# Kernel optimization log

Hardware: AMD Instinct MI355X
Metric: run time of the kernel (lower is better)

Reference implementation:

```python
import jax, jax.numpy as jnp
import numpy as np

HIDDEN = 1024
N_HEADS = 16
HEAD_DIM = HIDDEN // N_HEADS  # 64
B, N = 2, 2048
SCALE = HIDDEN ** (-0.5)  # NOTE: original scales by full hidden_size, not head_dim


def setup_inputs() -> dict:
    key = jax.random.key(0)
    k1, k2 = jax.random.split(key)
    hidden_states = jax.random.normal(k1, (B, N, HIDDEN), dtype=jnp.float32)
    attention_mask = jnp.ones((B, N), dtype=jnp.int32)
    # per-head no-bias Linear(hidden -> 3*head_dim), stacked: [h, hidden, 3*head_dim]
    W_qkv = jax.random.normal(k2, (N_HEADS, HIDDEN, 3 * HEAD_DIM), dtype=jnp.float32) * (HIDDEN ** -0.5)
    return {"hidden_states": hidden_states, "attention_mask": attention_mask, "W_qkv": W_qkv}


def reference(hidden_states, attention_mask, W_qkv):
    # qkv: [b, h, n, 3*d]
    qkv = jnp.einsum('bnD,hDe->bhne', hidden_states, W_qkv)
    q, k, v = jnp.split(qkv, 3, axis=-1)  # each [b, h, n, d]
    scores = jnp.einsum('bhid,bhjd->bhij', q, k) * SCALE
    mask = attention_mask[:, None, None, :] == 0  # [b,1,1,n]
    scores = jnp.where(mask, -jnp.inf, scores)
    attn = jax.nn.softmax(scores, axis=-1)
    out = jnp.einsum('bhij,bhjd->bhid', attn, v)  # [b, h, n, d]
    # rearrange 'b h n d -> b n (h d)'
    return jnp.transpose(out, (0, 2, 1, 3)).reshape(out.shape[0], out.shape[2], -1)
```

## Files before the change

kernel.cpp:

```cpp
#include <hip/hip_runtime.h>
#include <hip/hip_bf16.h>


#define NH   16
#define HD   64
#define SEQ  2048
#define HID  1024
#define E3   192
#define QSCALE 0.04508422017f
#define MBIAS  -43.2808512f

typedef __attribute__((ext_vector_type(8))) short short8;
typedef __attribute__((ext_vector_type(4))) float f32x4;
typedef __attribute__((ext_vector_type(16))) float f32x16;
typedef unsigned short ushort_t;

#define MFMA16(a, b, c) __builtin_amdgcn_mfma_f32_16x16x32_bf16((a), (b), (c), 0, 0, 0)
#define MFMA32(a, b, c) __builtin_amdgcn_mfma_f32_32x32x16_bf16((a), (b), (c), 0, 0, 0)

#if __has_builtin(__builtin_amdgcn_exp2f)
#define EXP2(x) __builtin_amdgcn_exp2f(x)
#else
#define EXP2(x) exp2f(x)
#endif

static __device__ __forceinline__ ushort_t f2bf(float x) {
    unsigned u = __builtin_bit_cast(unsigned, x);
    unsigned r = u + 0x7fff + ((u >> 16) & 1);
    return (ushort_t)(r >> 16);
}

static __device__ __forceinline__ unsigned pack_trunc(float hi, float lo) {
#if __has_builtin(__builtin_amdgcn_perm)
    return __builtin_amdgcn_perm(__builtin_bit_cast(unsigned, hi),
                                 __builtin_bit_cast(unsigned, lo), 0x07060302u);
#else
    return (__builtin_bit_cast(unsigned, hi) & 0xffff0000u) |
           (__builtin_bit_cast(unsigned, lo) >> 16);
#endif
}

static __device__ __forceinline__ void load_lds16(const void* g, void* l) {
    __builtin_amdgcn_global_load_lds(
        (__attribute__((address_space(1))) void*)(g),
        (__attribute__((address_space(3))) void*)(l), 16, 0, 0);
}

__global__ __launch_bounds__(256) void k_cvt_x(const void* __restrict__ Xv,
                                               ushort_t* __restrict__ Xb,
                                               int* __restrict__ flagp) {
    __shared__ int cnt;
    if (threadIdx.x == 0) cnt = 0;
    __syncthreads();
    const unsigned* X32 = (const unsigned*)Xv;
    if (threadIdx.x < 64) {
        unsigned u = X32[(size_t)blockIdx.x * 2048 + threadIdx.x * 32 + 7];
        int bexp = (u >> 7) & 0xFF;
        if (bexp >= 0x68 && bexp <= 0x90) atomicAdd(&cnt, 1);
    }
    __syncthreads();
    const int isf32 = (cnt < 32);
    if (blockIdx.x == 0 && threadIdx.x == 0) *flagp = isf32;

    const size_t base = ((size_t)blockIdx.x * 256 + threadIdx.x) * 16;
    if (isf32) {
        const float* Xf = (const float*)Xv;
        ushort_t tmp[16];
#pragma unroll
        for (int c = 0; c < 4; ++c) {
            float4 v = *(const float4*)(Xf + base + c * 4);
            tmp[c * 4 + 0] = f2bf(v.x); tmp[c * 4 + 1] = f2bf(v.y);
            tmp[c * 4 + 2] = f2bf(v.z); tmp[c * 4 + 3] = f2bf(v.w);
        }
        *(float4*)(Xb + base)     = ((const float4*)tmp)[0];
        *(float4*)(Xb + base + 8) = ((const float4*)tmp)[1];
    } else {
        const ushort_t* Xh = (const ushort_t*)Xv;
        *(float4*)(Xb + base)     = *(const float4*)(Xh + base);
        *(float4*)(Xb + base + 8) = *(const float4*)(Xh + base + 8);
    }
}

__global__ __launch_bounds__(256) void k_cvt_w(const void* __restrict__ Wv,
                                               ushort_t* __restrict__ Wt,
                                               const int* __restrict__ flagp) {
    __shared__ ushort_t tile[64][72];
    const int isf32 = *flagp;
    const int h  = blockIdx.x;
    const int dt = blockIdx.y;
    const int et = blockIdx.z;
    const int D0 = dt * 64, e0 = et * 64;
    const int t  = threadIdx.x;
#pragma unroll
    for (int r = 0; r < 2; ++r) {
        int row = r * 32 + (t >> 3);
        int col = (t & 7) * 8;
        size_t base = ((size_t)(h * HID + D0 + row)) * E3 + e0 + col;
        if (isf32) {
            const float* Wf = (const float*)Wv;
            float4 a = *(const float4*)(Wf + base);
            float4 c = *(const float4*)(Wf + base + 4);
            tile[row][col + 0] = f2bf(a.x); tile[row][col + 1] = f2bf(a.y);
            tile[row][col + 2] = f2bf(a.z); tile[row][col + 3] = f2bf(a.w);
            tile[row][col + 4] = f2bf(c.x); tile[row][col + 5] = f2bf(c.y);
            tile[row][col + 6] = f2bf(c.z); tile[row][col + 7] = f2bf(c.w);
        } else {
            *(float4*)&tile[row][col] = *(const float4*)((const ushort_t*)Wv + base);
        }
    }
    __syncthreads();
#pragma unroll
    for (int r = 0; r < 2; ++r) {
        int erow = r * 32 + (t >> 3);
        int dcol = (t & 7) * 8;
        ushort_t vals[8];
#pragma unroll
        for (int i = 0; i < 8; ++i) vals[i] = tile[dcol + i][erow];
        *(float4*)(Wt + ((size_t)(h * E3 + e0 + erow)) * HID + D0 + dcol) = *(float4*)vals;
    }
}

__global__ __launch_bounds__(256) void k_qkv(const ushort_t* __restrict__ Xb,
                                             const ushort_t* __restrict__ Wt,
                                             ushort_t* __restrict__ Qb,
                                             ushort_t* __restrict__ Kb,
                                             ushort_t* __restrict__ Vtb) {
    __shared__ __align__(16) ushort_t smem[2 * 128 * 64];
    ushort_t* Xl = smem;
    ushort_t* Wl = smem + 128 * 64;

    const int e0 = blockIdx.x * 128;
    const int m0 = blockIdx.y * 128;
    const int b  = m0 >> 11;
    const int n0 = m0 & 2047;
    const int t = threadIdx.x;
    const int w = t >> 6, lane = t & 63, l15 = lane & 15, quad = lane >> 4;
    const int wrow0 = (w & 1) * 64, wcol0 = (w >> 1) * 64;
    const int srow = lane >> 3;
    const int scb  = (lane & 7) ^ srow;

    f32x4 acc[4][4];
#pragma unroll
    for (int i = 0; i < 4; ++i)
#pragma unroll
        for (int j = 0; j < 4; ++j) acc[i][j] = (f32x4){0.f, 0.f, 0.f, 0.f};

    for (int k0 = 0; k0 < HID; k0 += 64) {
        __syncthreads();
#pragma unroll
        for (int cc = 0; cc < 4; ++cc) {
            const int ch  = w * 4 + cc;
            const int row = ch * 8 + srow;
            load_lds16(Xb + (size_t)(m0 + row) * HID + k0 + scb * 8, &Xl[ch * 512]);
            load_lds16(Wt + (size_t)(e0 + row) * HID + k0 + scb * 8, &Wl[ch * 512]);
        }
        __syncthreads();
#pragma unroll
        for (int kh = 0; kh < 2; ++kh) {
            short8 af[4], bfm[4];
#pragma unroll
            for (int i = 0; i < 4; ++i) {
                const int r = wrow0 + i * 16 + l15;
                af[i] = *(const short8*)&Xl[r * 64 + ((kh * 4 + quad) ^ (r & 7)) * 8];
            }
#pragma unroll
            for (int j = 0; j < 4; ++j) {
                const int r = wcol0 + j * 16 + l15;
                bfm[j] = *(const short8*)&Wl[r * 64 + ((kh * 4 + quad) ^ (r & 7)) * 8];
            }
#pragma unroll
            for (int i = 0; i < 4; ++i)
#pragma unroll
                for (int j = 0; j < 4; ++j)
                    acc[i][j] = MFMA16(af[i], bfm[j], acc[i][j]);
        }
    }

    ushort_t* Vbuf = smem;
    __syncthreads();
#pragma unroll
    for (int i = 0; i < 4; ++i) {
#pragma unroll
        for (int j = 0; j < 4; ++j) {
            const int E0v = e0 + wcol0 + j * 16;
            const int hh  = E0v / 192;
            const int r0  = E0v - hh * 192;
            const int bh  = b * NH + hh;
            const int nb  = n0 + wrow0 + i * 16 + quad * 4;
            if (r0 < 64) {
                const int e = r0 + l15;
#pragma unroll
                for (int reg = 0; reg < 4; ++reg)
                    Qb[((size_t)bh * SEQ + nb + reg) * HD + e] = f2bf(acc[i][j][reg] * QSCALE);
            } else if (r0 < 128) {
                const int e = r0 - 64 + l15;
#pragma unroll
                for (int reg = 0; reg < 4; ++reg)
                    Kb[((size_t)bh * SEQ + nb + reg) * HD + e] = f2bf(acc[i][j][reg]);
            } else {
                const int d  = r0 - 128 + l15;
                const int nl = wrow0 + i * 16 + quad * 4;
#pragma unroll
                for (int reg = 0; reg < 4; ++reg)
                    Vbuf[d * 136 + nl + reg] = f2bf(acc[i][j][reg]);
            }
        }
    }
    const int m3 = blockIdx.x % 3;
    if (m3 != 0) {
        __syncthreads();
        const int hv  = (e0 + ((m3 == 1) ? 0 : 64)) / 192;
        const int bhv = b * NH + hv;
        const int dr = t >> 2, part = t & 3;
        size_t dst = ((size_t)bhv * HD + dr) * SEQ + n0 + part * 32;
#pragma unroll
        for (int c = 0; c < 4; ++c) {
            float4 v = *(const float4*)&Vbuf[dr * 136 + part * 32 + c * 8];
            *(float4*)(Vtb + dst + c * 8) = v;
        }
    }
}


#define SMPACK(sv, h0v, h1v)                                                  \
    {                                                                         \
        _Pragma("unroll")                                                     \
        for (int g = 0; g < 4; ++g) {                                         \
            float p0 = EXP2(sv[4*g+0]); float p1 = EXP2(sv[4*g+1]);           \
            float p2 = EXP2(sv[4*g+2]); float p3 = EXP2(sv[4*g+3]);           \
            l_r += (p0 + p1) + (p2 + p3);                                     \
            unsigned a0 = pack_trunc(p1, p0), a1 = pack_trunc(p3, p2);        \
            unsigned b0 = a0, b1 = a1;                                        \
            asm volatile("v_permlane32_swap_b32 %0, %1" : "+v"(a0), "+v"(b0));\
            asm volatile("v_permlane32_swap_b32 %0, %1" : "+v"(a1), "+v"(b1));\
            h0v[g*2+0] = a0; h1v[g*2+0] = b0;                                 \
            h0v[g*2+1] = a1; h1v[g*2+1] = b1;                                 \
        }                                                                     \
    }

#define MAKE_PB(dst, h0v, h1v, GB)                                            \
    {                                                                         \
        unsigned w0_ = hi ? h0v[(GB+1)*2+0] : h0v[(GB)*2+0];                  \
        unsigned w1_ = hi ? h0v[(GB+1)*2+1] : h0v[(GB)*2+1];                  \
        unsigned w2_ = hi ? h1v[(GB+1)*2+0] : h1v[(GB)*2+0];                  \
        unsigned w3_ = hi ? h1v[(GB+1)*2+1] : h1v[(GB)*2+1];                  \
        uint4 u_ = {w0_, w1_, w2_, w3_};                                      \
        dst = __builtin_bit_cast(short8, u_);                                 \
    }

__global__ __launch_bounds__(256) void k_attn(const ushort_t* __restrict__ Qb,
                                              const ushort_t* __restrict__ Kb,
                                              const ushort_t* __restrict__ Vtb,
                                              const int* __restrict__ mask,
                                              void* __restrict__ outv,
                                              const int* __restrict__ flagp) {
    __shared__ __align__(16) char smem_raw[57344];
    float* biasl = (float*)(smem_raw + 49152);

    const int isf32 = *flagp;
    const int q0 = blockIdx.x * 128;
    const int bh = blockIdx.y;
    const int b  = bh >> 4, h = bh & 15;
    const int t  = threadIdx.x;
    const int w  = t >> 6, lane = t & 63;
    const int c31 = lane & 31, hi = lane >> 5;
    const int srow = lane >> 3;
    const int scb  = (lane & 7) ^ srow;
    const int rx7  = c31 & 7;

#pragma unroll
    for (int tj = 0; tj < 2; ++tj) {
        ushort_t* kb = (ushort_t*)(smem_raw + tj * 16384);
        ushort_t* vb = kb + 4096;
        load_lds16(Kb  + ((size_t)bh * SEQ + tj * 64 + w * 16 + srow)     * HD + scb * 8, &kb[(w * 2 + 0) * 512]);
        load_lds16(Kb  + ((size_t)bh * SEQ + tj * 64 + w * 16 + 8 + srow) * HD + scb * 8, &kb[(w * 2 + 1) * 512]);
        load_lds16(Vtb + ((size_t)bh * HD + w * 16 + srow)     * SEQ + tj * 64 + scb * 8, &vb[(w * 2 + 0) * 512]);
        load_lds16(Vtb + ((size_t)bh * HD + w * 16 + 8 + srow) * SEQ + tj * 64 + scb * 8, &vb[(w * 2 + 1) * 512]);
    }

    int lm = 0;
    for (int i = t; i < SEQ; i += 256) {
        int mv = mask[b * SEQ + i];
        biasl[i] = mv ? 0.0f : MBIAS;
        lm |= (mv == 0);
    }
    const int qrow = q0 + w * 32 + c31;
    short8 qB[4];
#pragma unroll
    for (int ds = 0; ds < 4; ++ds)
        qB[ds] = *(const short8*)(Qb + ((size_t)bh * SEQ + qrow) * HD + ds * 16 + hi * 8);

    const int use_bias = __syncthreads_or(lm);

    f32x16 oa, ob;
#pragma unroll
    for (int i = 0; i < 16; ++i) { oa[i] = 0.f; ob[i] = 0.f; }
    float l_r = 0.f;

    for (int j0 = 0; j0 < SEQ; j0 += 64) {
        const int idx = (j0 >> 6) % 3;
        if (j0 + 64 < SEQ) { asm volatile("s_waitcnt vmcnt(4)" ::: "memory"); }
        else               { asm volatile("s_waitcnt vmcnt(0)" ::: "memory"); }
        __builtin_amdgcn_s_barrier();
        asm volatile("" ::: "memory");
        if (j0 + 128 < SEQ) {
            ushort_t* kb2 = (ushort_t*)(smem_raw + ((idx + 2) % 3) * 16384);
            ushort_t* vb2 = kb2 + 4096;
            load_lds16(Kb  + ((size_t)bh * SEQ + j0 + 128 + w * 16 + srow)     * HD + scb * 8, &kb2[(w * 2 + 0) * 512]);
            load_lds16(Kb  + ((size_t)bh * SEQ + j0 + 128 + w * 16 + 8 + srow) * HD + scb * 8, &kb2[(w * 2 + 1) * 512]);
            load_lds16(Vtb + ((size_t)bh * HD + w * 16 + srow)     * SEQ + j0 + 128 + scb * 8, &vb2[(w * 2 + 0) * 512]);
            load_lds16(Vtb + ((size_t)bh * HD + w * 16 + 8 + srow) * SEQ + j0 + 128 + scb * 8, &vb2[(w * 2 + 1) * 512]);
        }
        ushort_t* kb = (ushort_t*)(smem_raw + idx * 16384);
        ushort_t* vb = kb + 4096;

        f32x16 s0, s1;
#pragma unroll
        for (int i = 0; i < 16; ++i) { s0[i] = 0.f; s1[i] = 0.f; }
#pragma unroll
        for (int ds = 0; ds < 4; ++ds) {
            short8 kf0 = *(const short8*)&kb[(c31)      * 64 + ((2 * ds + hi) ^ rx7) * 8];
            short8 kf1 = *(const short8*)&kb[(32 + c31) * 64 + ((2 * ds + hi) ^ rx7) * 8];
            s0 = MFMA32(kf0, qB[ds], s0);
            s1 = MFMA32(kf1, qB[ds], s1);
        }
        if (use_bias) {
#pragma unroll
            for (int g = 0; g < 4; ++g) {
                float4 bj0 = *(const float4*)&biasl[j0 +      8 * g + 4 * hi];
                float4 bj1 = *(const float4*)&biasl[j0 + 32 + 8 * g + 4 * hi];
                s0[4*g+0] += bj0.x; s0[4*g+1] += bj0.y; s0[4*g+2] += bj0.z; s0[4*g+3] += bj0.w;
                s1[4*g+0] += bj1.x; s1[4*g+1] += bj1.y; s1[4*g+2] += bj1.z; s1[4*g+3] += bj1.w;
            }
        }

        unsigned h0a[8], h1a[8], h0b[8], h1b[8];
        SMPACK(s0, h0a, h1a);
        SMPACK(s1, h0b, h1b);

#pragma unroll
        for (int jt = 0; jt < 2; ++jt) {
#pragma unroll
            for (int c13 = 0; c13 < 2; ++c13) {
                short8 pb;
                if (jt == 0) { MAKE_PB(pb, h0a, h1a, 2 * c13); }
                else         { MAKE_PB(pb, h0b, h1b, 2 * c13); }
                const int cbase = 2 * (jt * 2 + c13) + hi;
                short8 va0 = *(const short8*)&vb[(c31)      * 64 + (cbase ^ rx7) * 8];
                short8 va1 = *(const short8*)&vb[(32 + c31) * 64 + (cbase ^ rx7) * 8];
                oa = MFMA32(va0, pb, oa);
                ob = MFMA32(va1, pb, ob);
            }
        }
    }

    l_r += __shfl_xor(l_r, 32);
    const float rinv = 1.0f / l_r;

    __syncthreads();
    const int qlr = w * 32 + c31;
    const int r = t >> 1, part = t & 1;
    if (!isf32) {
        ushort_t* Ol = (ushort_t*)smem_raw;
#pragma unroll
        for (int dt = 0; dt < 2; ++dt) {
            const f32x16 ov = dt ? ob : oa;
#pragma unroll
            for (int g = 0; g < 4; ++g) {
                const int d0 = dt * 32 + 8 * g + 4 * hi;
                uint2 u;
                u.x = (unsigned)f2bf(ov[4*g+0] * rinv) | ((unsigned)f2bf(ov[4*g+1] * rinv) << 16);
                u.y = (unsigned)f2bf(ov[4*g+2] * rinv) | ((unsigned)f2bf(ov[4*g+3] * rinv) << 16);
                *(uint2*)&Ol[qlr * 72 + d0] = u;
            }
        }
        __syncthreads();
        ushort_t* outp = (ushort_t*)outv;
        size_t dst = ((size_t)b * SEQ + q0 + r) * HID + h * HD + part * 32;
#pragma unroll
        for (int c = 0; c < 4; ++c)
            *(float4*)(outp + dst + c * 8) = *(const float4*)&Ol[r * 72 + part * 32 + c * 8];
    } else {
        float* Olf = (float*)smem_raw;
#pragma unroll
        for (int dt = 0; dt < 2; ++dt) {
            const f32x16 ov = dt ? ob : oa;
#pragma unroll
            for (int g = 0; g < 4; ++g) {
                const int d0 = dt * 32 + 8 * g + 4 * hi;
                float4 fv;
                fv.x = ov[4*g+0] * rinv; fv.y = ov[4*g+1] * rinv;
                fv.z = ov[4*g+2] * rinv; fv.w = ov[4*g+3] * rinv;
                *(float4*)&Olf[qlr * 68 + d0] = fv;
            }
        }
        __syncthreads();
        float* outp = (float*)outv;
        size_t dst = ((size_t)b * SEQ + q0 + r) * HID + h * HD + part * 32;
#pragma unroll
        for (int c = 0; c < 8; ++c)
            *(float4*)(outp + dst + c * 4) = *(const float4*)&Olf[r * 68 + part * 32 + c * 4];
    }
}

extern "C" void kernel_launch(void* const* d_in, const int* in_sizes, int n_in,
                              void* d_out, int out_size, void* d_ws, size_t ws_size,
                              hipStream_t stream) {
    const void* X    = d_in[0];
    const int*  mask = (const int*)d_in[1];
    const void* W    = d_in[2];

    char* ws = (char*)d_ws;
    ushort_t* Qb    = (ushort_t*)(ws);
    ushort_t* Kb    = (ushort_t*)(ws + 8388608);
    ushort_t* Vtb   = (ushort_t*)(ws + 16777216);
    ushort_t* Wtb   = (ushort_t*)(ws + 25165824);
    int*      flagp = (int*)(ws + 31457280);
    ushort_t* Xb    = (ushort_t*)d_out;

    k_cvt_x<<<1024, 256, 0, stream>>>(X, Xb, flagp);
    k_cvt_w<<<dim3(16, 16, 3), 256, 0, stream>>>(W, Wtb, flagp);
    k_qkv<<<dim3(24, 32), 256, 0, stream>>>(Xb, Wtb, Qb, Kb, Vtb);
    k_attn<<<dim3(16, 32), 256, 0, stream>>>(Qb, Kb, Vtb, mask, d_out, flagp);
}
```

Before: 186.6 us.

## Split attention key range across wave pairs with 512-thread blocks and LDS merge

Doubles the attention block to 512 threads. Each pair of waves shares a 32-row query tile and splits every 64-key chunk into two 32-key halves, so each wave issues half the QK and PV MFMAs per iteration. The partial outputs and row sums are combined through LDS before normalisation, and the K/V staging loads are redistributed across eight waves. This raises waves per CU and latency hiding, at the cost of an extra LDS reduction, more barriers, and register pressure under launch_bounds(512,4).

```diff
diff --git a/kernel.cpp b/kernel.cpp
--- a/kernel.cpp
+++ b/kernel.cpp
@@ -248,12 +248,12 @@
         dst = __builtin_bit_cast(short8, u_);                                 \
     }
 
-__global__ __launch_bounds__(256) void k_attn(const ushort_t* __restrict__ Qb,
-                                              const ushort_t* __restrict__ Kb,
-                                              const ushort_t* __restrict__ Vtb,
-                                              const int* __restrict__ mask,
-                                              void* __restrict__ outv,
-                                              const int* __restrict__ flagp) {
+__global__ __launch_bounds__(512, 4) void k_attn(const ushort_t* __restrict__ Qb,
+                                                 const ushort_t* __restrict__ Kb,
+                                                 const ushort_t* __restrict__ Vtb,
+                                                 const int* __restrict__ mask,
+                                                 void* __restrict__ outv,
+                                                 const int* __restrict__ flagp) {
     __shared__ __align__(16) char smem_raw[57344];
     float* biasl = (float*)(smem_raw + 49152);
 
@@ -263,6 +263,7 @@
     const int b  = bh >> 4, h = bh & 15;
     const int t  = threadIdx.x;
     const int w  = t >> 6, lane = t & 63;
+    const int wq = w >> 1, jh = w & 1;
     const int c31 = lane & 31, hi = lane >> 5;
     const int srow = lane >> 3;
     const int scb  = (lane & 7) ^ srow;
@@ -272,19 +273,17 @@
     for (int tj = 0; tj < 2; ++tj) {
         ushort_t* kb = (ushort_t*)(smem_raw + tj * 16384);
         ushort_t* vb = kb + 4096;
-        load_lds16(Kb  + ((size_t)bh * SEQ + tj * 64 + w * 16 + srow)     * HD + scb * 8, &kb[(w * 2 + 0) * 512]);
-        load_lds16(Kb  + ((size_t)bh * SEQ + tj * 64 + w * 16 + 8 + srow) * HD + scb * 8, &kb[(w * 2 + 1) * 512]);
-        load_lds16(Vtb + ((size_t)bh * HD + w * 16 + srow)     * SEQ + tj * 64 + scb * 8, &vb[(w * 2 + 0) * 512]);
-        load_lds16(Vtb + ((size_t)bh * HD + w * 16 + 8 + srow) * SEQ + tj * 64 + scb * 8, &vb[(w * 2 + 1) * 512]);
+        load_lds16(Kb  + ((size_t)bh * SEQ + tj * 64 + w * 8 + srow) * HD + scb * 8, &kb[w * 512]);
+        load_lds16(Vtb + ((size_t)bh * HD + w * 8 + srow) * SEQ + tj * 64 + scb * 8, &vb[w * 512]);
     }
 
     int lm = 0;
-    for (int i = t; i < SEQ; i += 256) {
+    for (int i = t; i < SEQ; i += 512) {
         int mv = mask[b * SEQ + i];
         biasl[i] = mv ? 0.0f : MBIAS;
         lm |= (mv == 0);
     }
-    const int qrow = q0 + w * 32 + c31;
+    const int qrow = q0 + wq * 32 + c31;
     short8 qB[4];
 #pragma unroll
     for (int ds = 0; ds < 4; ++ds)
@@ -292,114 +291,135 @@
 
     const int use_bias = __syncthreads_or(lm);
 
-    f32x16 oa, ob;
-#pragma unroll
-    for (int i = 0; i < 16; ++i) { oa[i] = 0.f; ob[i] = 0.f; }
+    const f32x16 z16 = {0.f,0.f,0.f,0.f,0.f,0.f,0.f,0.f,0.f,0.f,0.f,0.f,0.f,0.f,0.f,0.f};
+    f32x16 oa = z16, ob = z16;
     float l_r = 0.f;
+
+    const int jrow = jh * 32 + c31;
 
     for (int j0 = 0; j0 < SEQ; j0 += 64) {
         const int idx = (j0 >> 6) % 3;
-        if (j0 + 64 < SEQ) { asm volatile("s_waitcnt vmcnt(4)" ::: "memory"); }
+        if (j0 + 64 < SEQ) { asm volatile("s_waitcnt vmcnt(2)" ::: "memory"); }
         else               { asm volatile("s_waitcnt vmcnt(0)" ::: "memory"); }
         __builtin_amdgcn_s_barrier();
         asm volatile("" ::: "memory");
         if (j0 + 128 < SEQ) {
             ushort_t* kb2 = (ushort_t*)(smem_raw + ((idx + 2) % 3) * 16384);
             ushort_t* vb2 = kb2 + 4096;
-            load_lds16(Kb  + ((size_t)bh * SEQ + j0 + 128 + w * 16 + srow)     * HD + scb * 8, &kb2[(w * 2 + 0) * 512]);
-            load_lds16(Kb  + ((size_t)bh * SEQ + j0 + 128 + w * 16 + 8 + srow) * HD + scb * 8, &kb2[(w * 2 + 1) * 512]);
-            load_lds16(Vtb + ((size_t)bh * HD + w * 16 + srow)     * SEQ + j0 + 128 + scb * 8, &vb2[(w * 2 + 0) * 512]);
-            load_lds16(Vtb + ((size_t)bh * HD + w * 16 + 8 + srow) * SEQ + j0 + 128 + scb * 8, &vb2[(w * 2 + 1) * 512]);
+            load_lds16(Kb  + ((size_t)bh * SEQ + j0 + 128 + w * 8 + srow) * HD + scb * 8, &kb2[w * 512]);
+            load_lds16(Vtb + ((size_t)bh * HD + w * 8 + srow) * SEQ + j0 + 128 + scb * 8, &vb2[w * 512]);
         }
         ushort_t* kb = (ushort_t*)(smem_raw + idx * 16384);
         ushort_t* vb = kb + 4096;
 
-        f32x16 s0, s1;
-#pragma unroll
-        for (int i = 0; i < 16; ++i) { s0[i] = 0.f; s1[i] = 0.f; }
-#pragma unroll
-        for (int ds = 0; ds < 4; ++ds) {
-            short8 kf0 = *(const short8*)&kb[(c31)      * 64 + ((2 * ds + hi) ^ rx7) * 8];
-            short8 kf1 = *(const short8*)&kb[(32 + c31) * 64 + ((2 * ds + hi) ^ rx7) * 8];
-            s0 = MFMA32(kf0, qB[ds], s0);
-            s1 = MFMA32(kf1, qB[ds], s1);
+        short8 kf0 = *(const short8*)&kb[jrow * 64 + ((0 + hi) ^ rx7) * 8];
+        f32x16 s = MFMA32(kf0, qB[0], z16);
+#pragma unroll
+        for (int ds = 1; ds < 4; ++ds) {
+            short8 kf = *(const short8*)&kb[jrow * 64 + ((2 * ds + hi) ^ rx7) * 8];
+            s = MFMA32(kf, qB[ds], s);
         }
         if (use_bias) {
 #pragma unroll
             for (int g = 0; g < 4; ++g) {
-                float4 bj0 = *(const float4*)&biasl[j0 +      8 * g + 4 * hi];
-                float4 bj1 = *(const float4*)&biasl[j0 + 32 + 8 * g + 4 * hi];
-                s0[4*g+0] += bj0.x; s0[4*g+1] += bj0.y; s0[4*g+2] += bj0.z; s0[4*g+3] += bj0.w;
-                s1[4*g+0] += bj1.x; s1[4*g+1] += bj1.y; s1[4*g+2] += bj1.z; s1[4*g+3] += bj1.w;
-            }
-        }
-
-        unsigned h0a[8], h1a[8], h0b[8], h1b[8];
-        SMPACK(s0, h0a, h1a);
-        SMPACK(s1, h0b, h1b);
-
-#pragma unroll
-        for (int jt = 0; jt < 2; ++jt) {
-#pragma unroll
-            for (int c13 = 0; c13 < 2; ++c13) {
-                short8 pb;
-                if (jt == 0) { MAKE_PB(pb, h0a, h1a, 2 * c13); }
-                else         { MAKE_PB(pb, h0b, h1b, 2 * c13); }
-                const int cbase = 2 * (jt * 2 + c13) + hi;
-                short8 va0 = *(const short8*)&vb[(c31)      * 64 + (cbase ^ rx7) * 8];
-                short8 va1 = *(const short8*)&vb[(32 + c31) * 64 + (cbase ^ rx7) * 8];
-                oa = MFMA32(va0, pb, oa);
-                ob = MFMA32(va1, pb, ob);
-            }
-        }
-    }
-
-    l_r += __shfl_xor(l_r, 32);
-    const float rinv = 1.0f / l_r;
-
-    __syncthreads();
-    const int qlr = w * 32 + c31;
-    const int r = t >> 1, part = t & 1;
+                float4 bj = *(const float4*)&biasl[j0 + jh * 32 + 8 * g + 4 * hi];
+                s[4*g+0] += bj.x; s[4*g+1] += bj.y; s[4*g+2] += bj.z; s[4*g+3] += bj.w;
+            }
+        }
+
+        unsigned h0[8], h1[8];
+        SMPACK(s, h0, h1);
+
+#pragma unroll
+        for (int c13 = 0; c13 < 2; ++c13) {
+            short8 pb;
+            MAKE_PB(pb, h0, h1, 2 * c13);
+            const int cbase = 2 * (jh * 2 + c13) + hi;
+            short8 va0 = *(const short8*)&vb[(c31)      * 64 + (cbase ^ rx7) * 8];
+            short8 va1 = *(const short8*)&vb[(32 + c31) * 64 + (cbase ^ rx7) * 8];
+            oa = MFMA32(va0, pb, oa);
+            ob = MFMA32(va1, pb, ob);
+        }
+    }
+
+    float l_h = l_r + __shfl_xor(l_r, 32);
+
+    __syncthreads();
+    float* Obuf = (float*)smem_raw;
+    float* Lbuf = (float*)(smem_raw + 49152);
+    const int slot = (wq * 64 + lane) * 36;
+    if (jh == 1) {
+#pragma unroll
+        for (int g = 0; g < 4; ++g) {
+            *(float4*)&Obuf[slot + g * 4]      = (float4){oa[4*g], oa[4*g+1], oa[4*g+2], oa[4*g+3]};
+            *(float4*)&Obuf[slot + 16 + g * 4] = (float4){ob[4*g], ob[4*g+1], ob[4*g+2], ob[4*g+3]};
+        }
+        Lbuf[wq * 64 + lane] = l_h;
+    }
+    __syncthreads();
+    float rinv = 0.f;
+    if (jh == 0) {
+        const float l_tot = l_h + Lbuf[wq * 64 + lane];
+        rinv = 1.0f / l_tot;
+#pragma unroll
+        for (int g = 0; g < 4; ++g) {
+            float4 pa = *(const float4*)&Obuf[slot + g * 4];
+            float4 pb4 = *(const float4*)&Obuf[slot + 16 + g * 4];
+            oa[4*g] += pa.x; oa[4*g+1] += pa.y; oa[4*g+2] += pa.z; oa[4*g+3] += pa.w;
+            ob[4*g] += pb4.x; ob[4*g+1] += pb4.y; ob[4*g+2] += pb4.z; ob[4*g+3] += pb4.w;
+        }
+    }
+    __syncthreads();
+
+    const int qlr = wq * 32 + c31;
+    const int r = t >> 2, part = t & 3;
     if (!isf32) {
         ushort_t* Ol = (ushort_t*)smem_raw;
-#pragma unroll
-        for (int dt = 0; dt < 2; ++dt) {
-            const f32x16 ov = dt ? ob : oa;
-#pragma unroll
-            for (int g = 0; g < 4; ++g) {
-                const int d0 = dt * 32 + 8 * g + 4 * hi;
-                uint2 u;
-                u.x = (unsigned)f2bf(ov[4*g+0] * rinv) | ((unsigned)f2bf(ov[4*g+1] * rinv) << 16);
-                u.y = (unsigned)f2bf(ov[4*g+2] * rinv) | ((unsigned)f2bf(ov[4*g+3] * rinv) << 16);
-                *(uint2*)&Ol[qlr * 72 + d0] = u;
+        if (jh == 0) {
+#pragma unroll
+            for (int dt = 0; dt < 2; ++dt) {
+                const f32x16 ov = dt ? ob : oa;
+#pragma unroll
+                for (int g = 0; g < 4; ++g) {
+                    const int d0 = dt * 32 + 8 * g + 4 * hi;
+                    uint2 u;
+                    u.x = (unsigned)f2bf(ov[4*g+0] * rinv) | ((unsigned)f2bf(ov[4*g+1] * rinv) << 16);
+                    u.y = (unsigned)f2bf(ov[4*g+2] * rinv) | ((unsigned)f2bf(ov[4*g+3] * rinv) << 16);
+                    *(uint2*)&Ol[qlr * 72 + d0] = u;
+                }
             }
         }
         __syncthreads();
         ushort_t* outp = (ushort_t*)outv;
-        size_t dst = ((size_t)b * SEQ + q0 + r) * HID + h * HD + part * 32;
-#pragma unroll
-        for (int c = 0; c < 4; ++c)
-            *(float4*)(outp + dst + c * 8) = *(const float4*)&Ol[r * 72 + part * 32 + c * 8];
+        size_t dst = ((size_t)b * SEQ + q0 + r) * HID + h * HD + part * 16;
+        float4 v0 = *(const float4*)&Ol[r * 72 + part * 16];
+        float4 v1 = *(const float4*)&Ol[r * 72 + part * 16 + 8];
+        *(float4*)(outp + dst)     = v0;
+        *(float4*)(outp + dst + 8) = v1;
     } else {
         float* Olf = (float*)smem_raw;
-#pragma unroll
-        for (int dt = 0; dt < 2; ++dt) {
-            const f32x16 ov = dt ? ob : oa;
-#pragma unroll
-            for (int g = 0; g < 4; ++g) {
-                const int d0 = dt * 32 + 8 * g + 4 * hi;
-                float4 fv;
-                fv.x = ov[4*g+0] * rinv; fv.y = ov[4*g+1] * rinv;
-                fv.z = ov[4*g+2] * rinv; fv.w = ov[4*g+3] * rinv;
-                *(float4*)&Olf[qlr * 68 + d0] = fv;
+        if (jh == 0) {
+#pragma unroll
+            for (int dt = 0; dt < 2; ++dt) {
+                const f32x16 ov = dt ? ob : oa;
+#pragma unroll
+                for (int g = 0; g < 4; ++g) {
+                    const int d0 = dt * 32 + 8 * g + 4 * hi;
+                    float4 fv;
+                    fv.x = ov[4*g+0] * rinv; fv.y = ov[4*g+1] * rinv;
+                    fv.z = ov[4*g+2] * rinv; fv.w = ov[4*g+3] * rinv;
+                    *(float4*)&Olf[qlr * 68 + d0] = fv;
+                }
             }
         }
         __syncthreads();
         float* outp = (float*)outv;
-        size_t dst = ((size_t)b * SEQ + q0 + r) * HID + h * HD + part * 32;
-#pragma unroll
-        for (int c = 0; c < 8; ++c)
-            *(float4*)(outp + dst + c * 4) = *(const float4*)&Olf[r * 68 + part * 32 + c * 4];
+        size_t dst = ((size_t)b * SEQ + q0 + r) * HID + h * HD + part * 16;
+#pragma unroll
+        for (int c = 0; c < 4; ++c) {
+            float4 v = *(const float4*)&Olf[r * 68 + part * 16 + c * 4];
+            *(float4*)(outp + dst + c * 4) = v;
+        }
     }
 }
 
@@ -421,5 +441,5 @@
     k_cvt_x<<<1024, 256, 0, stream>>>(X, Xb, flagp);
     k_cvt_w<<<dim3(16, 16, 3), 256, 0, stream>>>(W, Wtb, flagp);
     k_qkv<<<dim3(24, 32), 256, 0, stream>>>(Xb, Wtb, Qb, Kb, Vtb);
-    k_attn<<<dim3(16, 32), 256, 0, stream>>>(Qb, Kb, Vtb, mask, d_out, flagp);
-}
+    k_attn<<<dim3(16, 32), 512, 0, stream>>>(Qb, Kb, Vtb, mask, d_out, flagp);
+}
```

After: 175.3 us. 1.06x faster.
